# Performance work log

Hardware: AMD Instinct MI355X
Metric: run time of the kernel (lower is better)

The kernel has to match this reference:

```python
import jax, jax.numpy as jnp
import numpy as np

AUDIO_DIM, TEXT_DIM, HIDDEN_DIM = 512, 768, 512
B, AUDIO_LEN, TEXT_LEN = 8, 2048, 512


def setup_inputs() -> dict:
    key = jax.random.key(0)
    ks = jax.random.split(key, 9)
    audio_features = jax.random.normal(ks[0], (B, AUDIO_LEN, AUDIO_DIM), dtype=jnp.float32)
    text_features = jax.random.normal(ks[1], (B, TEXT_LEN, TEXT_DIM), dtype=jnp.float32)
    text_mask = jax.random.randint(ks[2], (B, TEXT_LEN), 0, 2).astype(jnp.int32)
    # Linear params (PyTorch default init scale ~ U(-1/sqrt(fan_in), 1/sqrt(fan_in)))
    def lin(kw, kb, fan_in, fan_out):
        bound = 1.0 / np.sqrt(fan_in)
        W = jax.random.uniform(kw, (fan_in, fan_out), minval=-bound, maxval=bound, dtype=jnp.float32)
        b = jax.random.uniform(kb, (fan_out,), minval=-bound, maxval=bound, dtype=jnp.float32)
        return W, b
    Wq, bq = lin(ks[3], ks[4], AUDIO_DIM, HIDDEN_DIM)
    Wk, bk = lin(ks[5], ks[6], TEXT_DIM, HIDDEN_DIM)
    Wv, bv = lin(ks[7], ks[8], TEXT_DIM, HIDDEN_DIM)
    return {
        "audio_features": audio_features,
        "text_features": text_features,
        "Wq": Wq, "bq": bq, "Wk": Wk, "bk": bk, "Wv": Wv, "bv": bv,
        "text_mask": text_mask,
    }


def reference(audio_features, text_features, Wq, bq, Wk, bk, Wv, bv, text_mask):
    scale = HIDDEN_DIM ** -0.5
    q = jnp.einsum("bad,dh->bah", audio_features, Wq) + bq  # (B, A, H)
    k = jnp.einsum("btd,dh->bth", text_features, Wk) + bk   # (B, T, H)
    v = jnp.einsum("btd,dh->bth", text_features, Wv) + bv   # (B, T, H)
    scores = jnp.einsum("bah,bth->bat", q, k) * scale        # (B, A, T)
    mask = text_mask[:, None, :]  # (B, 1, T)
    scores = jnp.where(mask == 0, -jnp.inf, scores)
    attn = jax.nn.softmax(scores, axis=-1)
    # dropout is identity in eval mode
    enhanced_audio = jnp.einsum("bat,bth->bah", attn, v)     # (B, A, H)
    return enhanced_audio
```

## Files before the change

### kernel.cpp

```cpp
#include <hip/hip_runtime.h>
#include <cstdint>
#include <cstddef>

#define AUDIO_DIM 512
#define TEXT_DIM  768
#define HIDDEN    512
#define BATCH     8
#define ALEN      2048
#define TLEN      512

typedef _Float16 half8 __attribute__((ext_vector_type(8)));
typedef _Float16 half4_t __attribute__((ext_vector_type(4)));
typedef float floatx4 __attribute__((ext_vector_type(4)));

#define AS1 __attribute__((address_space(1)))
#define AS3 __attribute__((address_space(3)))

__device__ __forceinline__ void gload_lds16(const void* g, void* l) {
    __builtin_amdgcn_global_load_lds((const AS1 void*)g, (AS3 void*)l, 16, 0, 0);
}

__device__ __forceinline__ int swz(int r) { return (r >> 1) & 3; }

__global__ __launch_bounds__(256) void prep(
    const float* __restrict__ audio, const float* __restrict__ text,
    const float* __restrict__ Wq, const float* __restrict__ Wk,
    const float* __restrict__ Wv,
    _Float16* __restrict__ audio_h, _Float16* __restrict__ text_h,
    _Float16* __restrict__ Wq_t, _Float16* __restrict__ Wk_t,
    _Float16* __restrict__ Wv_t)
{
    __shared__ _Float16 tt[32 * 33];
    const int bid = blockIdx.x, tid = threadIdx.x;
    if (bid < 11264) {
        const float* src; _Float16* dst; int i;
        if (bid < 8192) { src = audio; dst = audio_h; i = bid * 256 + tid; }
        else            { src = text;  dst = text_h;  i = (bid - 8192) * 256 + tid; }
        float4 v = ((const float4*)src)[i];
        half4_t h;
        h.x = (_Float16)v.x; h.y = (_Float16)v.y; h.z = (_Float16)v.z; h.w = (_Float16)v.w;
        ((half4_t*)dst)[i] = h;
    } else {
        const float* src; _Float16* dst; int R, lb;
        if (bid < 11520)      { lb = bid - 11264; src = Wq; dst = Wq_t; R = 512; }
        else if (bid < 11904) { lb = bid - 11520; src = Wk; dst = Wk_t; R = 768; }
        else                  { lb = bid - 11904; src = Wv; dst = Wv_t; R = 768; }
        const int C = 512;
        const int c0 = (lb & 15) * 32, r0 = (lb >> 4) * 32;
        const int tx = tid & 31, ty = tid >> 5;
#pragma unroll
        for (int i = 0; i < 4; i++) {
            int r = ty + i * 8;
            tt[r * 33 + tx] = (_Float16)src[(size_t)(r0 + r) * C + c0 + tx];
        }
        __syncthreads();
#pragma unroll
        for (int i = 0; i < 4; i++) {
            int r = ty + i * 8;
            dst[(size_t)(c0 + r) * R + r0 + tx] = tt[tx * 33 + r];
        }
    }
}

template <bool OUT16, bool ROWBIAS>
__device__ __forceinline__ void gemm_body(
    const _Float16* __restrict__ A, const _Float16* __restrict__ Bt,
    const float* __restrict__ bias, void* __restrict__ Cp,
    int N, int K, int m0, int n0, _Float16* Asm, _Float16* Bsm)
{
    const int tid = threadIdx.x;
    const int l = tid & 63, w = tid >> 6;
    const int wm = w >> 1, wn = w & 1;
    const int srow = l >> 2, sj = l & 3;
    const int q = l >> 4, c16 = l & 15;

    floatx4 acc[4][4] = {};

    for (int k0 = 0; k0 < K; k0 += 32) {
        if (k0) __syncthreads();
#pragma unroll
        for (int i = 0; i < 2; i++) {
            int rb = (w * 2 + i) * 16;
            int r = rb + srow;
            int cc = sj ^ swz(r);
            gload_lds16(A + (size_t)(m0 + r) * K + k0 + cc * 8, Asm + rb * 32);
            gload_lds16(Bt + (size_t)(n0 + r) * K + k0 + cc * 8, Bsm + rb * 32);
        }
        __syncthreads();

        half8 af[4], bf[4];
#pragma unroll
        for (int t = 0; t < 4; t++) {
            int rA = wm * 64 + t * 16 + c16;
            af[t] = *(const half8*)&Asm[rA * 32 + ((q ^ swz(rA)) << 3)];
            int rB = wn * 64 + t * 16 + c16;
            bf[t] = *(const half8*)&Bsm[rB * 32 + ((q ^ swz(rB)) << 3)];
        }
#pragma unroll
        for (int mi = 0; mi < 4; mi++)
#pragma unroll
            for (int ni = 0; ni < 4; ni++)
                acc[mi][ni] = __builtin_amdgcn_mfma_f32_16x16x32_f16(
                    af[mi], bf[ni], acc[mi][ni], 0, 0, 0);
    }

    if (OUT16) {
        float bcol[4];
        float brow[4][4];
        if (!ROWBIAS) {
#pragma unroll
            for (int ni = 0; ni < 4; ni++)
                bcol[ni] = bias[n0 + wn * 64 + ni * 16 + c16];
        } else {
#pragma unroll
            for (int mi = 0; mi < 4; mi++) {
                float4 b4 = *(const float4*)&bias[m0 + wm * 64 + mi * 16 + q * 4];
                brow[mi][0] = b4.x; brow[mi][1] = b4.y;
                brow[mi][2] = b4.z; brow[mi][3] = b4.w;
            }
        }
        _Float16* C = (_Float16*)Cp;
#pragma unroll
        for (int ni = 0; ni < 4; ni++) {
            int col = n0 + wn * 64 + ni * 16 + c16;
#pragma unroll
            for (int mi = 0; mi < 4; mi++) {
                int row = m0 + wm * 64 + mi * 16 + q * 4;
#pragma unroll
                for (int r = 0; r < 4; r++) {
                    float b = ROWBIAS ? brow[mi][r] : bcol[ni];
                    C[(size_t)(row + r) * N + col] = (_Float16)(acc[mi][ni][r] + b);
                }
            }
        }
    } else {
        float* C = (float*)Cp;
#pragma unroll
        for (int ni = 0; ni < 4; ni++) {
            int col = n0 + wn * 64 + ni * 16 + c16;
#pragma unroll
            for (int mi = 0; mi < 4; mi++) {
                int row = m0 + wm * 64 + mi * 16 + q * 4;
#pragma unroll
                for (int r = 0; r < 4; r++)
                    C[(size_t)(row + r) * N + col] = acc[mi][ni][r];
            }
        }
    }
}

__global__ __launch_bounds__(256, 3) void qkv_gemm(
    const _Float16* __restrict__ audio_h, const _Float16* __restrict__ text_h,
    const _Float16* __restrict__ Wq_t, const _Float16* __restrict__ Wk_t,
    const _Float16* __restrict__ Wv_t,
    const float* __restrict__ bq, const float* __restrict__ bk,
    const float* __restrict__ bv,
    _Float16* __restrict__ Qh, _Float16* __restrict__ Kh,
    _Float16* __restrict__ Vt)
{
    __shared__ __align__(16) _Float16 Asm[128 * 32];
    __shared__ __align__(16) _Float16 Bsm[128 * 32];
    const int bid = blockIdx.x;
    if (bid < 512) {
        int t = (bid & 7) * 64 + (bid >> 3);
        gemm_body<true, false>(audio_h, Wq_t, bq, Qh, 512, 512,
                               (t >> 2) * 128, (t & 3) * 128, Asm, Bsm);
    } else if (bid < 640) {
        int s = bid - 512;
        int t = (s & 7) * 16 + (s >> 3);
        gemm_body<true, false>(text_h, Wk_t, bk, Kh, 512, 768,
                               (t >> 2) * 128, (t & 3) * 128, Asm, Bsm);
    } else {
        int s = bid - 640;
        int t = (s & 7) * 16 + (s >> 3);
        int z = t >> 4, by = (t >> 2) & 3, bx = t & 3;
        gemm_body<true, true>(Wv_t, text_h + (size_t)z * 393216, bv,
                              Vt + (size_t)z * 262144, 512, 768,
                              by * 128, bx * 128, Asm, Bsm);
    }
}

__global__ __launch_bounds__(256, 2) void attn(
    const _Float16* __restrict__ Qh, const _Float16* __restrict__ Kh,
    const _Float16* __restrict__ Vt, const int* __restrict__ mask,
    float* __restrict__ out)
{
    __shared__ __align__(16) _Float16 Qs[32 * 512];
    __shared__ float red[4][32];
    __shared__ float red2[4][32];
    const int tid = threadIdx.x, l = tid & 63, w = tid >> 6;
    const int lin = blockIdx.x;
    const int tb = (lin & 7) * 64 + (lin >> 3);
    const int b = tb >> 6, a0 = (tb & 63) * 32;
    const _Float16* Qb = Qh + (size_t)(b * ALEN + a0) * HIDDEN;
    const _Float16* Kb = Kh + (size_t)b * TLEN * HIDDEN;
    const _Float16* Vb = Vt + (size_t)b * TLEN * HIDDEN;
    const int q = l >> 4, c16 = l & 15;

#pragma unroll
    for (int i = 0; i < 8; i++) {
        int r = w * 8 + i;
        gload_lds16(Qb + (size_t)r * 512 + ((l ^ (r & 7)) << 3), &Qs[r * 512]);
    }
    __syncthreads();

    floatx4 acc[2][8] = {};
#pragma unroll
    for (int ks = 0; ks < 16; ks++) {
        const int k0 = ks * 32;
        half8 af[2], bf[8];
#pragma unroll
        for (int t = 0; t < 2; t++) {
            int rA = t * 16 + c16;
            af[t] = *(const half8*)&Qs[rA * 512 + ((((k0 >> 3) + q) ^ (rA & 7)) << 3)];
        }
#pragma unroll
        for (int t = 0; t < 8; t++) {
            int rB = w * 128 + t * 16 + c16;
            bf[t] = *(const half8*)&Kb[(size_t)rB * 512 + k0 + q * 8];
        }
#pragma unroll
        for (int mi = 0; mi < 2; mi++)
#pragma unroll
            for (int ni = 0; ni < 8; ni++)
                acc[mi][ni] = __builtin_amdgcn_mfma_f32_16x16x32_f16(
                    af[mi], bf[ni], acc[mi][ni], 0, 0, 0);
    }

    const float scale = 0.044194173824159216f;
    int mv[8];
#pragma unroll
    for (int ni = 0; ni < 8; ni++)
        mv[ni] = mask[b * TLEN + w * 128 + ni * 16 + c16];
#pragma unroll
    for (int mi = 0; mi < 2; mi++)
#pragma unroll
        for (int ni = 0; ni < 8; ni++)
#pragma unroll
            for (int r = 0; r < 4; r++)
                acc[mi][ni][r] = mv[ni] ? acc[mi][ni][r] * scale : -1e30f;

    float mx[2][4];
#pragma unroll
    for (int mi = 0; mi < 2; mi++)
#pragma unroll
        for (int r = 0; r < 4; r++) {
            float m = -1e30f;
#pragma unroll
            for (int ni = 0; ni < 8; ni++) m = fmaxf(m, acc[mi][ni][r]);
#pragma unroll
            for (int off = 1; off <= 8; off <<= 1) m = fmaxf(m, __shfl_xor(m, off));
            mx[mi][r] = m;
        }
    if (c16 == 0)
#pragma unroll
        for (int mi = 0; mi < 2; mi++)
#pragma unroll
            for (int r = 0; r < 4; r++) red[w][mi * 16 + q * 4 + r] = mx[mi][r];
    __syncthreads();
#pragma unroll
    for (int mi = 0; mi < 2; mi++)
#pragma unroll
        for (int r = 0; r < 4; r++) {
            int row = mi * 16 + q * 4 + r;
            mx[mi][r] = fmaxf(fmaxf(red[0][row], red[1][row]),
                              fmaxf(red[2][row], red[3][row]));
        }

    float sm[2][4];
#pragma unroll
    for (int mi = 0; mi < 2; mi++)
#pragma unroll
        for (int r = 0; r < 4; r++) {
            float s = 0.f;
#pragma unroll
            for (int ni = 0; ni < 8; ni++) {
                float e = __expf(acc[mi][ni][r] - mx[mi][r]);
                acc[mi][ni][r] = e;
                s += e;
            }
#pragma unroll
            for (int off = 1; off <= 8; off <<= 1) s += __shfl_xor(s, off);
            sm[mi][r] = s;
        }
    if (c16 == 0)
#pragma unroll
        for (int mi = 0; mi < 2; mi++)
#pragma unroll
            for (int r = 0; r < 4; r++) red2[w][mi * 16 + q * 4 + r] = sm[mi][r];
    __syncthreads();
    _Float16* Ps = Qs;
#pragma unroll
    for (int mi = 0; mi < 2; mi++)
#pragma unroll
        for (int r = 0; r < 4; r++) {
            int row = mi * 16 + q * 4 + r;
            float inv = 1.f / (red2[0][row] + red2[1][row] + red2[2][row] + red2[3][row]);
#pragma unroll
            for (int ni = 0; ni < 8; ni++) {
                int col = w * 128 + ni * 16 + c16;
                Ps[row * 512 + ((((col >> 3) ^ (row & 7)) << 3) + (col & 7))] =
                    (_Float16)(acc[mi][ni][r] * inv);
            }
        }
    __syncthreads();

    floatx4 oacc[2][8] = {};
#pragma unroll
    for (int ts = 0; ts < 16; ts++) {
        const int t0 = ts * 32;
        half8 af[2], bf[8];
#pragma unroll
        for (int t = 0; t < 2; t++) {
            int rA = t * 16 + c16;
            af[t] = *(const half8*)&Ps[rA * 512 + ((((t0 >> 3) + q) ^ (rA & 7)) << 3)];
        }
#pragma unroll
        for (int h = 0; h < 8; h++) {
            int rB = w * 128 + h * 16 + c16;
            bf[h] = *(const half8*)&Vb[(size_t)rB * 512 + t0 + q * 8];
        }
#pragma unroll
        for (int mi = 0; mi < 2; mi++)
#pragma unroll
            for (int ni = 0; ni < 8; ni++)
                oacc[mi][ni] = __builtin_amdgcn_mfma_f32_16x16x32_f16(
                    af[mi], bf[ni], oacc[mi][ni], 0, 0, 0);
    }

    float* Ob = out + (size_t)(b * ALEN + a0) * HIDDEN;
#pragma unroll
    for (int ni = 0; ni < 8; ni++) {
        int col = w * 128 + ni * 16 + c16;
#pragma unroll
        for (int mi = 0; mi < 2; mi++) {
            int row = mi * 16 + q * 4;
#pragma unroll
            for (int r = 0; r < 4; r++)
                Ob[(size_t)(row + r) * HIDDEN + col] = oacc[mi][ni][r];
        }
    }
}

extern "C" void kernel_launch(void* const* d_in, const int* in_sizes, int n_in,
                              void* d_out, int out_size, void* d_ws, size_t ws_size,
                              hipStream_t stream)
{
    const float* audio = (const float*)d_in[0];
    const float* text  = (const float*)d_in[1];
    const float* Wq    = (const float*)d_in[2];
    const float* bq    = (const float*)d_in[3];
    const float* Wk    = (const float*)d_in[4];
    const float* bk    = (const float*)d_in[5];
    const float* Wv    = (const float*)d_in[6];
    const float* bv    = (const float*)d_in[7];
    const int*   maskp = (const int*)d_in[8];
    float* out = (float*)d_out;

    _Float16* audio_h = (_Float16*)d_out;
    _Float16* Qh      = audio_h + (size_t)8388608;

    _Float16* ws16   = (_Float16*)d_ws;
    _Float16* text_h = ws16;
    _Float16* Wq_t   = text_h + 3145728;
    _Float16* Wk_t   = Wq_t + 262144;
    _Float16* Wv_t   = Wk_t + 393216;
    _Float16* Kh     = Wv_t + 393216;
    _Float16* Vt     = Kh + 2097152;

    prep<<<12288, 256, 0, stream>>>(audio, text, Wq, Wk, Wv,
                                    audio_h, text_h, Wq_t, Wk_t, Wv_t);
    qkv_gemm<<<768, 256, 0, stream>>>(audio_h, text_h, Wq_t, Wk_t, Wv_t,
                                      bq, bk, bv, Qh, Kh, Vt);
    attn<<<512, 256, 0, stream>>>(Qh, Kh, Vt, maskp, out);
}
```

Baseline: 199.5 us.

## Stage K and V tiles through swizzled LDS instead of direct global loads

The attention kernel now streams 32-column slices of Q, K and V into shared memory with async global-to-LDS loads, synchronising between steps. The MFMA operands for K and V are then read from swizzled LDS, where before they were loaded straight from global memory. The aim is coalesced global access and lower global-load latency stalls. The cost is two barriers per k-step with no double buffering, and a larger LDS footprint (Q tile, 32 KB K/V tile, 32 KB P tile), which may limit the 2-blocks-per-CU occupancy.

```diff
diff --git a/kernel.cpp b/kernel.cpp
--- a/kernel.cpp
+++ b/kernel.cpp
@@ -185,7 +185,9 @@
     const _Float16* __restrict__ Vt, const int* __restrict__ mask,
     float* __restrict__ out)
 {
-    __shared__ __align__(16) _Float16 Qs[32 * 512];
+    __shared__ __align__(16) _Float16 Qs[32 * 32];
+    __shared__ __align__(16) _Float16 Ks[512 * 32];
+    __shared__ __align__(16) _Float16 Ps[32 * 512];
     __shared__ float red[4][32];
     __shared__ float red2[4][32];
     const int tid = threadIdx.x, l = tid & 63, w = tid >> 6;
@@ -195,29 +197,37 @@
     const _Float16* Qb = Qh + (size_t)(b * ALEN + a0) * HIDDEN;
     const _Float16* Kb = Kh + (size_t)b * TLEN * HIDDEN;
     const _Float16* Vb = Vt + (size_t)b * TLEN * HIDDEN;
+    const int srow = l >> 2, sj = l & 3;
     const int q = l >> 4, c16 = l & 15;
 
-#pragma unroll
-    for (int i = 0; i < 8; i++) {
-        int r = w * 8 + i;
-        gload_lds16(Qb + (size_t)r * 512 + ((l ^ (r & 7)) << 3), &Qs[r * 512]);
-    }
-    __syncthreads();
-
     floatx4 acc[2][8] = {};
-#pragma unroll
-    for (int ks = 0; ks < 16; ks++) {
-        const int k0 = ks * 32;
+    for (int k0 = 0; k0 < HIDDEN; k0 += 32) {
+        if (k0) __syncthreads();
+        if (w < 2) {
+            int rb = w * 16;
+            int r = rb + srow;
+            int cc = sj ^ swz(r);
+            gload_lds16(Qb + (size_t)r * HIDDEN + k0 + cc * 8, &Qs[rb * 32]);
+        }
+#pragma unroll
+        for (int i = 0; i < 8; i++) {
+            int rb = (w * 8 + i) * 16;
+            int r = rb + srow;
+            int cc = sj ^ swz(r);
+            gload_lds16(Kb + (size_t)r * HIDDEN + k0 + cc * 8, &Ks[rb * 32]);
+        }
+        __syncthreads();
+
         half8 af[2], bf[8];
 #pragma unroll
         for (int t = 0; t < 2; t++) {
             int rA = t * 16 + c16;
-            af[t] = *(const half8*)&Qs[rA * 512 + ((((k0 >> 3) + q) ^ (rA & 7)) << 3)];
+            af[t] = *(const half8*)&Qs[rA * 32 + ((q ^ swz(rA)) << 3)];
         }
 #pragma unroll
         for (int t = 0; t < 8; t++) {
             int rB = w * 128 + t * 16 + c16;
-            bf[t] = *(const half8*)&Kb[(size_t)rB * 512 + k0 + q * 8];
+            bf[t] = *(const half8*)&Ks[rB * 32 + ((q ^ swz(rB)) << 3)];
         }
 #pragma unroll
         for (int mi = 0; mi < 2; mi++)
@@ -289,7 +299,7 @@
 #pragma unroll
             for (int r = 0; r < 4; r++) red2[w][mi * 16 + q * 4 + r] = sm[mi][r];
     __syncthreads();
-    _Float16* Ps = Qs;
+
 #pragma unroll
     for (int mi = 0; mi < 2; mi++)
 #pragma unroll
@@ -306,9 +316,18 @@
     __syncthreads();
 
     floatx4 oacc[2][8] = {};
-#pragma unroll
     for (int ts = 0; ts < 16; ts++) {
         const int t0 = ts * 32;
+        if (ts) __syncthreads();
+#pragma unroll
+        for (int i = 0; i < 8; i++) {
+            int rb = (w * 8 + i) * 16;
+            int r = rb + srow;
+            int cc = sj ^ swz(r);
+            gload_lds16(Vb + (size_t)r * HIDDEN + t0 + cc * 8, &Ks[rb * 32]);
+        }
+        __syncthreads();
+
         half8 af[2], bf[8];
 #pragma unroll
         for (int t = 0; t < 2; t++) {
@@ -318,7 +337,7 @@
 #pragma unroll
         for (int h = 0; h < 8; h++) {
             int rB = w * 128 + h * 16 + c16;
-            bf[h] = *(const half8*)&Vb[(size_t)rB * 512 + t0 + q * 8];
+            bf[h] = *(const half8*)&Ks[rB * 32 + ((q ^ swz(rB)) << 3)];
         }
 #pragma unroll
         for (int mi = 0; mi < 2; mi++)
```

Result: faster. 175.6 us (-12.0%).

## Stage K and V tiles through LDS with async global-to-LDS pipelining in attention

Applied to the files above, without the earlier changes.

Replaces direct per-wave global loads of K and V fragments with async global_load_lds staging into a swizzled LDS buffer, split into two halves. The next k-slice half is prefetched while the current half feeds MFMAs, using manual vmcnt waits. The intent is to hide global memory latency in the QK^T and PV loops. It adds 32KB of LDS per block, which may reduce occupancy at two blocks per CU. The hand-placed waitcnt ordering also carries correctness risk, since each wave only writes and reads its own rows without block barriers.

```diff
diff --git a/kernel.cpp b/kernel.cpp
--- a/kernel.cpp
+++ b/kernel.cpp
@@ -21,6 +21,13 @@
 }
 
 __device__ __forceinline__ int swz(int r) { return (r >> 1) & 3; }
+
+#define VMCNT(N) asm volatile("s_waitcnt vmcnt(" #N ")" ::: "memory")
+#define LDS_REUSE_FENCE()                                   \
+    do {                                                    \
+        asm volatile("s_waitcnt lgkmcnt(0)" ::: "memory");  \
+        __builtin_amdgcn_sched_barrier(0);                  \
+    } while (0)
 
 __global__ __launch_bounds__(256) void prep(
     const float* __restrict__ audio, const float* __restrict__ text,
@@ -180,12 +187,26 @@
     }
 }
 
+
+#define STAGE_HALF(SRC, K0, H)                                              \
+    do {                                                                    \
+        _Pragma("unroll")                                                   \
+        for (int i_ = 0; i_ < 4; i_++) {                                    \
+            int rb_ = (w * 8 + (H) * 4 + i_) * 16;                          \
+            int r_ = rb_ + srow;                                            \
+            int cc_ = sj ^ swz(r_);                                         \
+            gload_lds16((SRC) + (size_t)r_ * HIDDEN + (K0) + cc_ * 8,       \
+                        &Ks[rb_ * 32]);                                     \
+        }                                                                   \
+    } while (0)
+
 __global__ __launch_bounds__(256, 2) void attn(
     const _Float16* __restrict__ Qh, const _Float16* __restrict__ Kh,
     const _Float16* __restrict__ Vt, const int* __restrict__ mask,
     float* __restrict__ out)
 {
-    __shared__ __align__(16) _Float16 Qs[32 * 512];
+    __shared__ __align__(16) _Float16 QPs[32 * 512];
+    __shared__ __align__(16) _Float16 Ks[512 * 32];
     __shared__ float red[4][32];
     __shared__ float red2[4][32];
     const int tid = threadIdx.x, l = tid & 63, w = tid >> 6;
@@ -195,36 +216,48 @@
     const _Float16* Qb = Qh + (size_t)(b * ALEN + a0) * HIDDEN;
     const _Float16* Kb = Kh + (size_t)b * TLEN * HIDDEN;
     const _Float16* Vb = Vt + (size_t)b * TLEN * HIDDEN;
+    const int srow = l >> 2, sj = l & 3;
     const int q = l >> 4, c16 = l & 15;
 
 #pragma unroll
     for (int i = 0; i < 8; i++) {
         int r = w * 8 + i;
-        gload_lds16(Qb + (size_t)r * 512 + ((l ^ (r & 7)) << 3), &Qs[r * 512]);
+        gload_lds16(Qb + (size_t)r * 512 + ((l ^ (r & 7)) << 3), &QPs[r * 512]);
     }
     __syncthreads();
 
     floatx4 acc[2][8] = {};
+    STAGE_HALF(Kb, 0, 0);
+    STAGE_HALF(Kb, 0, 1);
 #pragma unroll
     for (int ks = 0; ks < 16; ks++) {
         const int k0 = ks * 32;
-        half8 af[2], bf[8];
+        half8 af[2];
 #pragma unroll
         for (int t = 0; t < 2; t++) {
             int rA = t * 16 + c16;
-            af[t] = *(const half8*)&Qs[rA * 512 + ((((k0 >> 3) + q) ^ (rA & 7)) << 3)];
-        }
-#pragma unroll
-        for (int t = 0; t < 8; t++) {
-            int rB = w * 128 + t * 16 + c16;
-            bf[t] = *(const half8*)&Kb[(size_t)rB * 512 + k0 + q * 8];
-        }
-#pragma unroll
-        for (int mi = 0; mi < 2; mi++)
-#pragma unroll
-            for (int ni = 0; ni < 8; ni++)
-                acc[mi][ni] = __builtin_amdgcn_mfma_f32_16x16x32_f16(
-                    af[mi], bf[ni], acc[mi][ni], 0, 0, 0);
+            af[t] = *(const half8*)&QPs[rA * 512 + ((((k0 >> 3) + q) ^ (rA & 7)) << 3)];
+        }
+#pragma unroll
+        for (int h = 0; h < 2; h++) {
+            if (ks == 15 && h == 1) { VMCNT(0); } else { VMCNT(4); }
+            half8 bf[4];
+#pragma unroll
+            for (int t = 0; t < 4; t++) {
+                int rB = w * 128 + h * 64 + t * 16 + c16;
+                bf[t] = *(const half8*)&Ks[rB * 32 + ((q ^ swz(rB)) << 3)];
+            }
+#pragma unroll
+            for (int mi = 0; mi < 2; mi++)
+#pragma unroll
+                for (int t = 0; t < 4; t++)
+                    acc[mi][h * 4 + t] = __builtin_amdgcn_mfma_f32_16x16x32_f16(
+                        af[mi], bf[t], acc[mi][h * 4 + t], 0, 0, 0);
+            if (ks < 15) {
+                LDS_REUSE_FENCE();
+                STAGE_HALF(Kb, k0 + 32, h);
+            }
+        }
     }
 
     const float scale = 0.044194173824159216f;
@@ -289,7 +322,8 @@
 #pragma unroll
             for (int r = 0; r < 4; r++) red2[w][mi * 16 + q * 4 + r] = sm[mi][r];
     __syncthreads();
-    _Float16* Ps = Qs;
+
+    _Float16* Ps = QPs;
 #pragma unroll
     for (int mi = 0; mi < 2; mi++)
 #pragma unroll
@@ -306,26 +340,37 @@
     __syncthreads();
 
     floatx4 oacc[2][8] = {};
+    STAGE_HALF(Vb, 0, 0);
+    STAGE_HALF(Vb, 0, 1);
 #pragma unroll
     for (int ts = 0; ts < 16; ts++) {
         const int t0 = ts * 32;
-        half8 af[2], bf[8];
+        half8 af[2];
 #pragma unroll
         for (int t = 0; t < 2; t++) {
             int rA = t * 16 + c16;
             af[t] = *(const half8*)&Ps[rA * 512 + ((((t0 >> 3) + q) ^ (rA & 7)) << 3)];
         }
 #pragma unroll
-        for (int h = 0; h < 8; h++) {
-            int rB = w * 128 + h * 16 + c16;
-            bf[h] = *(const half8*)&Vb[(size_t)rB * 512 + t0 + q * 8];
-        }
-#pragma unroll
-        for (int mi = 0; mi < 2; mi++)
-#pragma unroll
-            for (int ni = 0; ni < 8; ni++)
-                oacc[mi][ni] = __builtin_amdgcn_mfma_f32_16x16x32_f16(
-                    af[mi], bf[ni], oacc[mi][ni], 0, 0, 0);
+        for (int h = 0; h < 2; h++) {
+            if (ts == 15 && h == 1) { VMCNT(0); } else { VMCNT(4); }
+            half8 bf[4];
+#pragma unroll
+            for (int t = 0; t < 4; t++) {
+                int rB = w * 128 + h * 64 + t * 16 + c16;
+                bf[t] = *(const half8*)&Ks[rB * 32 + ((q ^ swz(rB)) << 3)];
+            }
+#pragma unroll
+            for (int mi = 0; mi < 2; mi++)
+#pragma unroll
+                for (int t = 0; t < 4; t++)
+                    oacc[mi][h * 4 + t] = __builtin_amdgcn_mfma_f32_16x16x32_f16(
+                        af[mi], bf[t], oacc[mi][h * 4 + t], 0, 0, 0);
+            if (ts < 15) {
+                LDS_REUSE_FENCE();
+                STAGE_HALF(Vb, t0 + 32, h);
+            }
+        }
     }
 
     float* Ob = out + (size_t)(b * ALEN + a0) * HIDDEN;
```

After: 176.7 us. 1.13x faster.

## Enlarge attention tile to 64 rows and double-buffer K/V through LDS

Applied to the files above, without the earlier changes.

The attention kernel now handles 64 audio rows per block with 8 waves instead of 32 rows with 4 waves. Each wave stages its K and V slices into private double-buffered LDS tiles using direct global-to-LDS loads, gated by explicit vmcnt waits, instead of reading fragments straight from global memory. This halves K/V global traffic per output row and overlaps the next slice's load with the current MFMAs. In exchange, LDS use roughly doubles to about 132 KB per block, so only one block fits per CU and the grid is halved.

```diff
diff --git a/kernel.cpp b/kernel.cpp
--- a/kernel.cpp
+++ b/kernel.cpp
@@ -21,6 +21,8 @@
 }
 
 __device__ __forceinline__ int swz(int r) { return (r >> 1) & 3; }
+
+#define VMCNT(N) asm volatile("s_waitcnt vmcnt(" #N ")" ::: "memory")
 
 __global__ __launch_bounds__(256) void prep(
     const float* __restrict__ audio, const float* __restrict__ text,
@@ -180,101 +182,122 @@
     }
 }
 
-__global__ __launch_bounds__(256, 2) void attn(
+
+#define STAGE64(SRC, K0, BUF)                                               \
+    do {                                                                    \
+        _Pragma("unroll")                                                   \
+        for (int i_ = 0; i_ < 4; i_++) {                                    \
+            int lr_ = i_ * 16 + srow;                                       \
+            int cc_ = sj ^ swz(lr_);                                        \
+            gload_lds16((SRC) + (size_t)(w * 64 + lr_) * HIDDEN + (K0) + cc_ * 8, \
+                        &(BUF)[i_ * 512]);                                  \
+        }                                                                   \
+    } while (0)
+
+__global__ __launch_bounds__(512, 2) void attn(
     const _Float16* __restrict__ Qh, const _Float16* __restrict__ Kh,
     const _Float16* __restrict__ Vt, const int* __restrict__ mask,
     float* __restrict__ out)
 {
-    __shared__ __align__(16) _Float16 Qs[32 * 512];
-    __shared__ float red[4][32];
-    __shared__ float red2[4][32];
+    __shared__ __align__(16) _Float16 QPs[64 * 512];
+    __shared__ __align__(16) _Float16 Ks[8][2][64 * 32];
+    __shared__ float red[8][64];
+    __shared__ float red2[8][64];
     const int tid = threadIdx.x, l = tid & 63, w = tid >> 6;
     const int lin = blockIdx.x;
-    const int tb = (lin & 7) * 64 + (lin >> 3);
-    const int b = tb >> 6, a0 = (tb & 63) * 32;
+    const int tb = (lin & 7) * 32 + (lin >> 3);
+    const int b = tb >> 5, a0 = (tb & 31) * 64;
     const _Float16* Qb = Qh + (size_t)(b * ALEN + a0) * HIDDEN;
     const _Float16* Kb = Kh + (size_t)b * TLEN * HIDDEN;
     const _Float16* Vb = Vt + (size_t)b * TLEN * HIDDEN;
+    const int srow = l >> 2, sj = l & 3;
     const int q = l >> 4, c16 = l & 15;
+
+    int mv[4];
+#pragma unroll
+    for (int ni = 0; ni < 4; ni++)
+        mv[ni] = mask[b * TLEN + w * 64 + ni * 16 + c16];
 
 #pragma unroll
     for (int i = 0; i < 8; i++) {
         int r = w * 8 + i;
-        gload_lds16(Qb + (size_t)r * 512 + ((l ^ (r & 7)) << 3), &Qs[r * 512]);
-    }
+        gload_lds16(Qb + (size_t)r * 512 + ((l ^ (r & 7)) << 3), &QPs[r * 512]);
+    }
+    STAGE64(Kb, 0, Ks[w][0]);
+    STAGE64(Kb, 32, Ks[w][1]);
     __syncthreads();
 
-    floatx4 acc[2][8] = {};
+    floatx4 acc[4][4] = {};
 #pragma unroll
     for (int ks = 0; ks < 16; ks++) {
         const int k0 = ks * 32;
-        half8 af[2], bf[8];
-#pragma unroll
-        for (int t = 0; t < 2; t++) {
+        if (ks == 15) { VMCNT(0); } else { VMCNT(4); }
+        half8 af[4], bf[4];
+        const _Float16* kb = &Ks[w][ks & 1][0];
+#pragma unroll
+        for (int t = 0; t < 4; t++) {
             int rA = t * 16 + c16;
-            af[t] = *(const half8*)&Qs[rA * 512 + ((((k0 >> 3) + q) ^ (rA & 7)) << 3)];
-        }
-#pragma unroll
-        for (int t = 0; t < 8; t++) {
-            int rB = w * 128 + t * 16 + c16;
-            bf[t] = *(const half8*)&Kb[(size_t)rB * 512 + k0 + q * 8];
-        }
-#pragma unroll
-        for (int mi = 0; mi < 2; mi++)
-#pragma unroll
-            for (int ni = 0; ni < 8; ni++)
+            af[t] = *(const half8*)&QPs[rA * 512 + ((((k0 >> 3) + q) ^ (rA & 7)) << 3)];
+            bf[t] = *(const half8*)&kb[rA * 32 + ((q ^ swz(rA)) << 3)];
+        }
+#pragma unroll
+        for (int mi = 0; mi < 4; mi++)
+#pragma unroll
+            for (int ni = 0; ni < 4; ni++)
                 acc[mi][ni] = __builtin_amdgcn_mfma_f32_16x16x32_f16(
                     af[mi], bf[ni], acc[mi][ni], 0, 0, 0);
-    }
+        if (ks < 14) STAGE64(Kb, k0 + 64, Ks[w][ks & 1]);
+    }
+
+    STAGE64(Vb, 0, Ks[w][0]);
+    STAGE64(Vb, 32, Ks[w][1]);
 
     const float scale = 0.044194173824159216f;
-    int mv[8];
-#pragma unroll
-    for (int ni = 0; ni < 8; ni++)
-        mv[ni] = mask[b * TLEN + w * 128 + ni * 16 + c16];
-#pragma unroll
-    for (int mi = 0; mi < 2; mi++)
-#pragma unroll
-        for (int ni = 0; ni < 8; ni++)
+#pragma unroll
+    for (int mi = 0; mi < 4; mi++)
+#pragma unroll
+        for (int ni = 0; ni < 4; ni++)
 #pragma unroll
             for (int r = 0; r < 4; r++)
                 acc[mi][ni][r] = mv[ni] ? acc[mi][ni][r] * scale : -1e30f;
 
-    float mx[2][4];
-#pragma unroll
-    for (int mi = 0; mi < 2; mi++)
+    float mx[4][4];
+#pragma unroll
+    for (int mi = 0; mi < 4; mi++)
 #pragma unroll
         for (int r = 0; r < 4; r++) {
             float m = -1e30f;
 #pragma unroll
-            for (int ni = 0; ni < 8; ni++) m = fmaxf(m, acc[mi][ni][r]);
+            for (int ni = 0; ni < 4; ni++) m = fmaxf(m, acc[mi][ni][r]);
 #pragma unroll
             for (int off = 1; off <= 8; off <<= 1) m = fmaxf(m, __shfl_xor(m, off));
             mx[mi][r] = m;
         }
     if (c16 == 0)
 #pragma unroll
-        for (int mi = 0; mi < 2; mi++)
+        for (int mi = 0; mi < 4; mi++)
 #pragma unroll
             for (int r = 0; r < 4; r++) red[w][mi * 16 + q * 4 + r] = mx[mi][r];
     __syncthreads();
 #pragma unroll
-    for (int mi = 0; mi < 2; mi++)
+    for (int mi = 0; mi < 4; mi++)
 #pragma unroll
         for (int r = 0; r < 4; r++) {
             int row = mi * 16 + q * 4 + r;
-            mx[mi][r] = fmaxf(fmaxf(red[0][row], red[1][row]),
-                              fmaxf(red[2][row], red[3][row]));
-        }
-
-    float sm[2][4];
-#pragma unroll
-    for (int mi = 0; mi < 2; mi++)
+            float m = red[0][row];
+#pragma unroll
+            for (int ww = 1; ww < 8; ww++) m = fmaxf(m, red[ww][row]);
+            mx[mi][r] = m;
+        }
+
+    float sm[4][4];
+#pragma unroll
+    for (int mi = 0; mi < 4; mi++)
 #pragma unroll
         for (int r = 0; r < 4; r++) {
             float s = 0.f;
 #pragma unroll
-            for (int ni = 0; ni < 8; ni++) {
+            for (int ni = 0; ni < 4; ni++) {
                 float e = __expf(acc[mi][ni][r] - mx[mi][r]);
                 acc[mi][ni][r] = e;
                 s += e;
@@ -285,55 +308,58 @@
         }
     if (c16 == 0)
 #pragma unroll
-        for (int mi = 0; mi < 2; mi++)
+        for (int mi = 0; mi < 4; mi++)
 #pragma unroll
             for (int r = 0; r < 4; r++) red2[w][mi * 16 + q * 4 + r] = sm[mi][r];
     __syncthreads();
-    _Float16* Ps = Qs;
-#pragma unroll
-    for (int mi = 0; mi < 2; mi++)
+
+    _Float16* Ps = QPs;
+#pragma unroll
+    for (int mi = 0; mi < 4; mi++)
 #pragma unroll
         for (int r = 0; r < 4; r++) {
             int row = mi * 16 + q * 4 + r;
-            float inv = 1.f / (red2[0][row] + red2[1][row] + red2[2][row] + red2[3][row]);
-#pragma unroll
-            for (int ni = 0; ni < 8; ni++) {
-                int col = w * 128 + ni * 16 + c16;
+            float s = red2[0][row];
+#pragma unroll
+            for (int ww = 1; ww < 8; ww++) s += red2[ww][row];
+            float inv = 1.f / s;
+#pragma unroll
+            for (int ni = 0; ni < 4; ni++) {
+                int col = w * 64 + ni * 16 + c16;
                 Ps[row * 512 + ((((col >> 3) ^ (row & 7)) << 3) + (col & 7))] =
                     (_Float16)(acc[mi][ni][r] * inv);
             }
         }
     __syncthreads();
 
-    floatx4 oacc[2][8] = {};
+    floatx4 oacc[4][4] = {};
 #pragma unroll
     for (int ts = 0; ts < 16; ts++) {
         const int t0 = ts * 32;
-        half8 af[2], bf[8];
-#pragma unroll
-        for (int t = 0; t < 2; t++) {
+        if (ts == 15) { VMCNT(0); } else { VMCNT(4); }
+        half8 af[4], bf[4];
+        const _Float16* vb = &Ks[w][ts & 1][0];
+#pragma unroll
+        for (int t = 0; t < 4; t++) {
             int rA = t * 16 + c16;
             af[t] = *(const half8*)&Ps[rA * 512 + ((((t0 >> 3) + q) ^ (rA & 7)) << 3)];
-        }
-#pragma unroll
-        for (int h = 0; h < 8; h++) {
-            int rB = w * 128 + h * 16 + c16;
-            bf[h] = *(const half8*)&Vb[(size_t)rB * 512 + t0 + q * 8];
-        }
-#pragma unroll
-        for (int mi = 0; mi < 2; mi++)
-#pragma unroll
-            for (int ni = 0; ni < 8; ni++)
+            bf[t] = *(const half8*)&vb[rA * 32 + ((q ^ swz(rA)) << 3)];
+        }
+#pragma unroll
+        for (int mi = 0; mi < 4; mi++)
+#pragma unroll
+            for (int ni = 0; ni < 4; ni++)
                 oacc[mi][ni] = __builtin_amdgcn_mfma_f32_16x16x32_f16(
                     af[mi], bf[ni], oacc[mi][ni], 0, 0, 0);
+        if (ts < 14) STAGE64(Vb, t0 + 64, Ks[w][ts & 1]);
     }
 
     float* Ob = out + (size_t)(b * ALEN + a0) * HIDDEN;
 #pragma unroll
-    for (int ni = 0; ni < 8; ni++) {
-        int col = w * 128 + ni * 16 + c16;
-#pragma unroll
-        for (int mi = 0; mi < 2; mi++) {
+    for (int ni = 0; ni < 4; ni++) {
+        int col = w * 64 + ni * 16 + c16;
+#pragma unroll
+        for (int mi = 0; mi < 4; mi++) {
             int row = mi * 16 + q * 4;
 #pragma unroll
             for (int r = 0; r < 4; r++)
@@ -372,5 +398,5 @@
                                     audio_h, text_h, Wq_t, Wk_t, Wv_t);
     qkv_gemm<<<768, 256, 0, stream>>>(audio_h, text_h, Wq_t, Wk_t, Wv_t,
                                       bq, bk, bv, Qh, Kh, Vt);
-    attn<<<512, 256, 0, stream>>>(Qh, Kh, Vt, maskp, out);
-}
+    attn<<<256, 512, 0, stream>>>(Qh, Kh, Vt, maskp, out);
+}
```

Result: faster. 165.2 us (-17.2%).
